# Kernel optimization log

Hardware: AMD Instinct MI355X
Metric: run time of the kernel (lower is better)

The kernel has to match this reference:

```python
import jax, jax.numpy as jnp
import numpy as np

TAU = 0.07
MARGIN = 0.2
NUM_SPECIES = 64  # matches fill_max of species_ids


def _l2norm(x):
    return x / jnp.linalg.norm(x, axis=-1, keepdims=True)


def setup_inputs() -> dict:
    key = jax.random.key(0)
    k1, k2, k3 = jax.random.split(key, 3)
    B, D = 8192, 256
    species_embed = _l2norm(jax.random.normal(k1, (B, D), dtype=jnp.float32))
    text_embed = _l2norm(jax.random.normal(k2, (B, D), dtype=jnp.float32))
    species_ids = jax.random.randint(k3, (B,), 0, NUM_SPECIES, dtype=jnp.int32)
    return {"species_embed": species_embed, "text_embed": text_embed,
            "species_ids": species_ids}


def reference(species_embed, text_embed, species_ids):
    B = species_embed.shape[0]
    dtype = species_embed.dtype

    sim = species_embed @ text_embed.T                      # (B, B)
    same = species_ids[:, None] == species_ids[None, :]     # (B, B) bool, symmetric
    diag_sim = jnp.diagonal(sim)                            # (B,)

    # ---- intra-species symmetric InfoNCE (per-species CE, averaged over species)
    logits = sim / TAU
    neg_inf = jnp.finfo(dtype).min
    masked = jnp.where(same, logits, neg_inf)               # restrict to same-species cols
    diag_logit = diag_sim / TAU
    ce_v2t = jax.scipy.special.logsumexp(masked, axis=1) - diag_logit   # per-row CE
    ce_t2v = jax.scipy.special.logsumexp(masked.T, axis=1) - diag_logit # transpose: same mask is symmetric

    ones = jnp.ones((B,), dtype=dtype)
    counts = jax.ops.segment_sum(ones, species_ids, num_segments=NUM_SPECIES)          # group sizes
    seg_v2t = jax.ops.segment_sum(ce_v2t, species_ids, num_segments=NUM_SPECIES)
    seg_t2v = jax.ops.segment_sum(ce_t2v, species_ids, num_segments=NUM_SPECIES)
    valid_s = counts >= 2                                   # groups with <2 members skipped
    per_species = (seg_v2t + seg_t2v) / (2.0 * jnp.maximum(counts, 1.0))
    n_valid = jnp.maximum(jnp.sum(valid_s.astype(dtype)), 1.0)
    loss_infonce = jnp.sum(jnp.where(valid_s, per_species, 0.0)) / n_valid

    # ---- cross-species triplet (pos = mean same-species sim excl. self, neg = mean diff-species sim)
    same_f = same.astype(dtype)
    row_same_sum = jnp.sum(sim * same_f, axis=1)            # includes diagonal
    row_sum = jnp.sum(sim, axis=1)
    pos_cnt = jnp.sum(same_f, axis=1) - 1.0
    neg_cnt = B - jnp.sum(same_f, axis=1)
    pos_mean = (row_same_sum - diag_sim) / jnp.maximum(pos_cnt, 1.0)
    neg_mean = (row_sum - row_same_sum) / jnp.maximum(neg_cnt, 1.0)
    tri = jax.nn.relu(neg_mean - pos_mean + MARGIN)
    valid_i = (pos_cnt > 0) & (neg_cnt > 0)
    n_valid_i = jnp.maximum(jnp.sum(valid_i.astype(dtype)), 1.0)
    loss_triplet = jnp.sum(jnp.where(valid_i, tri, 0.0)) / n_valid_i

    return loss_infonce + loss_triplet
```

## Files before the change

kernel.cpp:

```cpp
#include <hip/hip_runtime.h>
#include <hip/hip_fp16.h>

#define TAU 0.07f
#define MARGIN 0.2f
#define NSPEC 64
#define BB 8192
#define DD 256

#define WS_SCALARS   0
#define WS_COUNTS    288
#define WS_OFFSETS   544
#define WS_LSEROW    1024
#define WS_LSECOL    33792
#define WS_TS        66560
#define WS_DIAG      132096
#define WS_MEMBER    164864
#define WS_T         197632
#define WS_TRI       198656
#define WS_ZERO_BYTES 132096

typedef _Float16 half8 __attribute__((ext_vector_type(8)));
typedef float float4v __attribute__((ext_vector_type(4)));
typedef unsigned int uint4v __attribute__((ext_vector_type(4)));

__device__ __forceinline__ uint4v pack8(float4 a, float4 b) {
  half8 h;
  h[0] = (_Float16)a.x; h[1] = (_Float16)a.y; h[2] = (_Float16)a.z; h[3] = (_Float16)a.w;
  h[4] = (_Float16)b.x; h[5] = (_Float16)b.y; h[6] = (_Float16)b.z; h[7] = (_Float16)b.w;
  return __builtin_bit_cast(uint4v, h);
}

__global__ void k1_all(const int* __restrict__ ids, int* counts_g, int* offsets_g,
                       int* memberList, float* scalars) {
  __shared__ int cnt[NSPEC];
  __shared__ int off[NSPEC];
  int tid = threadIdx.x;
  if (tid < NSPEC) cnt[tid] = 0;
  __syncthreads();
  int myS[8], myP[8];
  #pragma unroll
  for (int r = 0; r < 8; ++r) {
    int i = r * 1024 + tid;
    int s = ids[i];
    myS[r] = s;
    myP[r] = atomicAdd(&cnt[s], 1);
  }
  __syncthreads();
  if (tid < NSPEC) {
    int o = 0;
    for (int t = 0; t < NSPEC; ++t) o += (t < tid) ? cnt[t] : 0;
    off[tid] = o;
    offsets_g[tid] = o;
    int c = cnt[tid];
    counts_g[tid] = c;
    unsigned long long bv = __ballot(c >= 2);
    float nvi = (c >= 2 && c <= BB - 1) ? (float)c : 0.f;
    for (int o2 = 1; o2 < 64; o2 <<= 1) nvi += __shfl_xor(nvi, o2);
    if (tid == 0) {
      scalars[2] = (float)__popcll(bv);
      scalars[3] = nvi;
    }
  }
  __syncthreads();
  #pragma unroll
  for (int r = 0; r < 8; ++r) {
    int i = r * 1024 + tid;
    memberList[off[myS[r]] + myP[r]] = i;
  }
}

__global__ void k2_ts(const float* __restrict__ tx, const int* __restrict__ counts,
                      const int* __restrict__ offsets, const int* __restrict__ memberList,
                      float* Ts) {
  int s = blockIdx.x, r = blockIdx.y;
  int m = counts[s], g0 = offsets[s];
  int k0 = (m * r) >> 3, k1 = (m * (r + 1)) >> 3;
  if (k0 >= k1) return;
  int d = threadIdx.x;
  float acc = 0.f;
  for (int k = k0; k < k1; ++k) acc += tx[memberList[g0 + k] * DD + d];
  atomicAdd(&Ts[s * DD + d], acc);
}

__global__ void k2b_t(const float* __restrict__ Ts, float* T) {
  int d = threadIdx.x;
  float acc = 0.f;
  for (int s = 0; s < NSPEC; ++s) acc += Ts[s * DD + d];
  T[d] = acc;
}

__global__ void k4_rows(const float* __restrict__ sp, const float* __restrict__ tx,
                        const int* __restrict__ ids, const int* __restrict__ counts,
                        const float* __restrict__ Ts, const float* __restrict__ T,
                        float* diag, float* tri) {
  int gt = blockIdx.x * 256 + threadIdx.x;
  int i = gt >> 6, lane = gt & 63;
  float4 a = *reinterpret_cast<const float4*>(sp + i * DD + lane * 4);
  float4 b = *reinterpret_cast<const float4*>(tx + i * DD + lane * 4);
  float4 tv = *reinterpret_cast<const float4*>(T + lane * 4);
  int s = ids[i];
  int m = counts[s];
  float4 c = *reinterpret_cast<const float4*>(Ts + s * DD + lane * 4);
  float dDiag = a.x * b.x + a.y * b.y + a.z * b.z + a.w * b.w;
  float dT    = a.x * tv.x + a.y * tv.y + a.z * tv.z + a.w * tv.w;
  float dTs   = a.x * c.x + a.y * c.y + a.z * c.z + a.w * c.w;
  #pragma unroll
  for (int o = 1; o < 64; o <<= 1) {
    dDiag += __shfl_xor(dDiag, o);
    dT    += __shfl_xor(dT, o);
    dTs   += __shfl_xor(dTs, o);
  }
  if (lane == 0) {
    diag[i] = dDiag;
    float posMean = (dTs - dDiag) / fmaxf((float)(m - 1), 1.f);
    float negMean = (dT - dTs) / fmaxf((float)(BB - m), 1.f);
    float t = fmaxf(negMean - posMean + MARGIN, 0.f);
    tri[i] = (m >= 2 && m <= BB - 1) ? t : 0.f;
  }
}

__global__ void k5_lse(const float* __restrict__ sp, const float* __restrict__ tx,
                       const int* __restrict__ counts, const int* __restrict__ offsets,
                       const int* __restrict__ memberList,
                       float* lseRow, float* lseCol) {
  __shared__ uint4v lds5[1536];
  int s = blockIdx.x;
  int m = counts[s];
  int g0 = offsets[s];
  int tid = threadIdx.x;
  int lane = tid & 63, wv = tid >> 6;
  int quad = lane >> 4, cl = lane & 15;

  for (int rt = blockIdx.y; rt * 64 < m; rt += gridDim.y) {
    for (int ct = blockIdx.z; ct * 128 < m; ct += gridDim.z) {
      float4v acc[8];
      #pragma unroll
      for (int cf = 0; cf < 8; ++cf) acc[cf] = (float4v){0.f, 0.f, 0.f, 0.f};

      for (int kc = 0; kc < 4; ++kc) {
        __syncthreads();
        #pragma unroll
        for (int p = 0; p < 6; ++p) {
          int u = p * 256 + tid;
          int isB = u >= 512;
          int v = isB ? (u - 512) : u;
          int row = v >> 3;
          int sub = v & 7;
          int ksl = sub >> 2, q = sub & 3;
          int d0 = kc * 64 + ksl * 32 + q * 8;
          int idx = isB ? (ct * 128 + row) : (rt * 64 + row);
          uint4v val = (uint4v){0u, 0u, 0u, 0u};
          if (idx < m) {
            const float* src = (isB ? tx : sp) + memberList[g0 + idx] * DD + d0;
            float4 f0 = *reinterpret_cast<const float4*>(src);
            float4 f1 = *reinterpret_cast<const float4*>(src + 4);
            val = pack8(f0, f1);
          }
          int dst = isB ? (512 + (ksl * 128 + row) * 4 + q)
                        : ((ksl * 64 + row) * 4 + q);
          lds5[dst] = val;
        }
        __syncthreads();
        #pragma unroll
        for (int ksl = 0; ksl < 2; ++ksl) {
          half8 a = __builtin_bit_cast(half8, lds5[(ksl * 64 + wv * 16 + cl) * 4 + quad]);
          #pragma unroll
          for (int cf = 0; cf < 8; ++cf) {
            half8 b = __builtin_bit_cast(half8, lds5[512 + (ksl * 128 + cf * 16 + cl) * 4 + quad]);
            acc[cf] = __builtin_amdgcn_mfma_f32_16x16x32_f16(a, b, acc[cf], 0, 0, 0);
          }
        }
      }

      int riBase = rt * 64 + wv * 16 + quad * 4;
      float rowAcc[4] = {0.f, 0.f, 0.f, 0.f};
      #pragma unroll
      for (int cf = 0; cf < 8; ++cf) {
        int ci = ct * 128 + cf * 16 + cl;
        bool cv = ci < m;
        float colAcc = 0.f;
        #pragma unroll
        for (int reg = 0; reg < 4; ++reg) {
          bool rv = (riBase + reg) < m;
          float e = (rv && cv) ? __expf(acc[cf][reg] * (1.f / TAU)) : 0.f;
          rowAcc[reg] += e;
          colAcc += e;
        }
        colAcc += __shfl_xor(colAcc, 16);
        colAcc += __shfl_xor(colAcc, 32);
        if (quad == 0 && cv) atomicAdd(&lseCol[g0 + ci], colAcc);
      }
      #pragma unroll
      for (int reg = 0; reg < 4; ++reg) {
        float v = rowAcc[reg];
        v += __shfl_xor(v, 1);
        v += __shfl_xor(v, 2);
        v += __shfl_xor(v, 4);
        v += __shfl_xor(v, 8);
        if (cl == 0 && (riBase + reg) < m) atomicAdd(&lseRow[g0 + riBase + reg], v);
      }
    }
  }
}

__global__ void k6_info(const int* __restrict__ memberList, const int* __restrict__ ids,
                        const int* __restrict__ counts, const float* __restrict__ lseRow,
                        const float* __restrict__ lseCol, const float* __restrict__ diag,
                        const float* __restrict__ tri, float* scalars) {
  __shared__ float red[8];
  int g = blockIdx.x * blockDim.x + threadIdx.x;
  int i = memberList[g];
  int s = ids[i];
  int m = counts[s];
  float tt = tri[i];
  float term = 0.f;
  if (m >= 2) {
    term = (__logf(lseRow[g]) + __logf(lseCol[g]) - 2.f * diag[i] * (1.f / TAU)) /
           (2.f * (float)m);
  }
  #pragma unroll
  for (int o = 1; o < 64; o <<= 1) {
    term += __shfl_xor(term, o);
    tt += __shfl_xor(tt, o);
  }
  int wv = threadIdx.x >> 6, lane = threadIdx.x & 63;
  if (lane == 0) { red[wv] = term; red[4 + wv] = tt; }
  __syncthreads();
  if (threadIdx.x == 0) {
    atomicAdd(&scalars[1], red[0] + red[1] + red[2] + red[3]);
    atomicAdd(&scalars[0], red[4] + red[5] + red[6] + red[7]);
  }
}

__global__ void k7_final(const float* __restrict__ scalars, float* out) {
  out[0] = scalars[1] / fmaxf(scalars[2], 1.f) + scalars[0] / fmaxf(scalars[3], 1.f);
}

extern "C" void kernel_launch(void* const* d_in, const int* in_sizes, int n_in,
                              void* d_out, int out_size, void* d_ws, size_t ws_size,
                              hipStream_t stream) {
  const float* sp = (const float*)d_in[0];
  const float* tx = (const float*)d_in[1];
  const int* ids = (const int*)d_in[2];
  float* out = (float*)d_out;

  char* ws = (char*)d_ws;
  float* scalars = (float*)(ws + WS_SCALARS);
  int* counts = (int*)(ws + WS_COUNTS);
  int* offsets = (int*)(ws + WS_OFFSETS);
  float* lseRow = (float*)(ws + WS_LSEROW);
  float* lseCol = (float*)(ws + WS_LSECOL);
  float* Ts = (float*)(ws + WS_TS);
  float* diag = (float*)(ws + WS_DIAG);
  int* memberList = (int*)(ws + WS_MEMBER);
  float* T = (float*)(ws + WS_T);
  float* tri = (float*)(ws + WS_TRI);

  hipMemsetAsync(d_ws, 0, WS_ZERO_BYTES, stream);
  k1_all<<<1, 1024, 0, stream>>>(ids, counts, offsets, memberList, scalars);
  k2_ts<<<dim3(NSPEC, 8), 256, 0, stream>>>(tx, counts, offsets, memberList, Ts);
  k2b_t<<<1, 256, 0, stream>>>(Ts, T);
  k4_rows<<<BB / 4, 256, 0, stream>>>(sp, tx, ids, counts, Ts, T, diag, tri);
  k5_lse<<<dim3(NSPEC, 4, 2), 256, 0, stream>>>(sp, tx, counts, offsets, memberList,
                                                lseRow, lseCol);
  k6_info<<<32, 256, 0, stream>>>(memberList, ids, counts, lseRow, lseCol, diag, tri,
                                  scalars);
  k7_final<<<1, 1, 0, stream>>>(scalars, out);
}
```

Baseline: 111.0 us.

## Fuse pipeline stages to cut kernel launches and the workspace memset

The workspace zeroing moves into the single-block k1 kernel, replacing the separate memset. The total-sum kernel is folded into k2_ts via atomic adds into T. The row-stats kernel and the LSE tile kernel are merged into one heterogeneous grid, with the LSE part remapped onto 128 blocks. The final scalar combine now runs in the last-arriving block of the info kernel through an atomic counter. This removes several launches and inter-kernel gaps, at the cost of extra global atomics and a serial zero-fill done by one block.

```diff
diff --git a/kernel.cpp b/kernel.cpp
--- a/kernel.cpp
+++ b/kernel.cpp
@@ -13,15 +13,18 @@
 #define WS_LSEROW    1024
 #define WS_LSECOL    33792
 #define WS_TS        66560
-#define WS_DIAG      132096
-#define WS_MEMBER    164864
-#define WS_T         197632
-#define WS_TRI       198656
-#define WS_ZERO_BYTES 132096
+#define WS_T         132096
+#define WS_ZERO_BYTES 133120
+#define WS_DIAG      133632
+#define WS_MEMBER    166400
+#define WS_TRI       199168
 
 typedef _Float16 half8 __attribute__((ext_vector_type(8)));
 typedef float float4v __attribute__((ext_vector_type(4)));
 typedef unsigned int uint4v __attribute__((ext_vector_type(4)));
+
+#define NB5 128
+#define NB45 (NB5 + BB/4)
 
 __device__ __forceinline__ uint4v pack8(float4 a, float4 b) {
   half8 h;
@@ -30,11 +33,14 @@
   return __builtin_bit_cast(uint4v, h);
 }
 
-__global__ void k1_all(const int* __restrict__ ids, int* counts_g, int* offsets_g,
-                       int* memberList, float* scalars) {
+__global__ void k1_all(const int* __restrict__ ids, char* ws, int* counts_g,
+                       int* offsets_g, int* memberList, float* scalars) {
   __shared__ int cnt[NSPEC];
   __shared__ int off[NSPEC];
   int tid = threadIdx.x;
+  float4* z = (float4*)ws;
+  float4 z4 = make_float4(0.f, 0.f, 0.f, 0.f);
+  for (int u = tid; u < WS_ZERO_BYTES / 16; u += 1024) z[u] = z4;
   if (tid < NSPEC) cnt[tid] = 0;
   __syncthreads();
   int myS[8], myP[8];
@@ -71,7 +77,7 @@
 
 __global__ void k2_ts(const float* __restrict__ tx, const int* __restrict__ counts,
                       const int* __restrict__ offsets, const int* __restrict__ memberList,
-                      float* Ts) {
+                      float* Ts, float* T) {
   int s = blockIdx.x, r = blockIdx.y;
   int m = counts[s], g0 = offsets[s];
   int k0 = (m * r) >> 3, k1 = (m * (r + 1)) >> 3;
@@ -80,59 +86,54 @@
   float acc = 0.f;
   for (int k = k0; k < k1; ++k) acc += tx[memberList[g0 + k] * DD + d];
   atomicAdd(&Ts[s * DD + d], acc);
-}
-
-__global__ void k2b_t(const float* __restrict__ Ts, float* T) {
-  int d = threadIdx.x;
-  float acc = 0.f;
-  for (int s = 0; s < NSPEC; ++s) acc += Ts[s * DD + d];
-  T[d] = acc;
-}
-
-__global__ void k4_rows(const float* __restrict__ sp, const float* __restrict__ tx,
-                        const int* __restrict__ ids, const int* __restrict__ counts,
-                        const float* __restrict__ Ts, const float* __restrict__ T,
-                        float* diag, float* tri) {
-  int gt = blockIdx.x * 256 + threadIdx.x;
-  int i = gt >> 6, lane = gt & 63;
-  float4 a = *reinterpret_cast<const float4*>(sp + i * DD + lane * 4);
-  float4 b = *reinterpret_cast<const float4*>(tx + i * DD + lane * 4);
-  float4 tv = *reinterpret_cast<const float4*>(T + lane * 4);
-  int s = ids[i];
-  int m = counts[s];
-  float4 c = *reinterpret_cast<const float4*>(Ts + s * DD + lane * 4);
-  float dDiag = a.x * b.x + a.y * b.y + a.z * b.z + a.w * b.w;
-  float dT    = a.x * tv.x + a.y * tv.y + a.z * tv.z + a.w * tv.w;
-  float dTs   = a.x * c.x + a.y * c.y + a.z * c.z + a.w * c.w;
-  #pragma unroll
-  for (int o = 1; o < 64; o <<= 1) {
-    dDiag += __shfl_xor(dDiag, o);
-    dT    += __shfl_xor(dT, o);
-    dTs   += __shfl_xor(dTs, o);
-  }
-  if (lane == 0) {
-    diag[i] = dDiag;
-    float posMean = (dTs - dDiag) / fmaxf((float)(m - 1), 1.f);
-    float negMean = (dT - dTs) / fmaxf((float)(BB - m), 1.f);
-    float t = fmaxf(negMean - posMean + MARGIN, 0.f);
-    tri[i] = (m >= 2 && m <= BB - 1) ? t : 0.f;
-  }
-}
-
-__global__ void k5_lse(const float* __restrict__ sp, const float* __restrict__ tx,
-                       const int* __restrict__ counts, const int* __restrict__ offsets,
-                       const int* __restrict__ memberList,
-                       float* lseRow, float* lseCol) {
+  atomicAdd(&T[d], acc);
+}
+
+__global__ void k45(const float* __restrict__ sp, const float* __restrict__ tx,
+                    const int* __restrict__ ids, const int* __restrict__ counts,
+                    const int* __restrict__ offsets, const int* __restrict__ memberList,
+                    const float* __restrict__ Ts, const float* __restrict__ T,
+                    float* diag, float* tri, float* lseRow, float* lseCol) {
   __shared__ uint4v lds5[1536];
-  int s = blockIdx.x;
+  int tid = threadIdx.x;
+
+  if (blockIdx.x >= NB5) {
+    int gt = (blockIdx.x - NB5) * 256 + tid;
+    int i = gt >> 6, lane = gt & 63;
+    float4 a = *reinterpret_cast<const float4*>(sp + i * DD + lane * 4);
+    float4 b = *reinterpret_cast<const float4*>(tx + i * DD + lane * 4);
+    float4 tv = *reinterpret_cast<const float4*>(T + lane * 4);
+    int s = ids[i];
+    int m = counts[s];
+    float4 c = *reinterpret_cast<const float4*>(Ts + s * DD + lane * 4);
+    float dDiag = a.x * b.x + a.y * b.y + a.z * b.z + a.w * b.w;
+    float dT    = a.x * tv.x + a.y * tv.y + a.z * tv.z + a.w * tv.w;
+    float dTs   = a.x * c.x + a.y * c.y + a.z * c.z + a.w * c.w;
+    #pragma unroll
+    for (int o = 1; o < 64; o <<= 1) {
+      dDiag += __shfl_xor(dDiag, o);
+      dT    += __shfl_xor(dT, o);
+      dTs   += __shfl_xor(dTs, o);
+    }
+    if (lane == 0) {
+      diag[i] = dDiag;
+      float posMean = (dTs - dDiag) / fmaxf((float)(m - 1), 1.f);
+      float negMean = (dT - dTs) / fmaxf((float)(BB - m), 1.f);
+      float t = fmaxf(negMean - posMean + MARGIN, 0.f);
+      tri[i] = (m >= 2 && m <= BB - 1) ? t : 0.f;
+    }
+    return;
+  }
+
+  int s = blockIdx.x >> 1;
+  int rt0 = blockIdx.x & 1;
   int m = counts[s];
   int g0 = offsets[s];
-  int tid = threadIdx.x;
   int lane = tid & 63, wv = tid >> 6;
   int quad = lane >> 4, cl = lane & 15;
 
-  for (int rt = blockIdx.y; rt * 64 < m; rt += gridDim.y) {
-    for (int ct = blockIdx.z; ct * 128 < m; ct += gridDim.z) {
+  for (int rt = rt0; rt * 64 < m; rt += 2) {
+    for (int ct = 0; ct * 128 < m; ++ct) {
       float4v acc[8];
       #pragma unroll
       for (int cf = 0; cf < 8; ++cf) acc[cf] = (float4v){0.f, 0.f, 0.f, 0.f};
@@ -203,10 +204,10 @@
   }
 }
 
-__global__ void k6_info(const int* __restrict__ memberList, const int* __restrict__ ids,
-                        const int* __restrict__ counts, const float* __restrict__ lseRow,
-                        const float* __restrict__ lseCol, const float* __restrict__ diag,
-                        const float* __restrict__ tri, float* scalars) {
+__global__ void k67_info(const int* __restrict__ memberList, const int* __restrict__ ids,
+                         const int* __restrict__ counts, const float* __restrict__ lseRow,
+                         const float* __restrict__ lseCol, const float* __restrict__ diag,
+                         const float* __restrict__ tri, float* scalars, float* out) {
   __shared__ float red[8];
   int g = blockIdx.x * blockDim.x + threadIdx.x;
   int i = memberList[g];
@@ -229,11 +230,14 @@
   if (threadIdx.x == 0) {
     atomicAdd(&scalars[1], red[0] + red[1] + red[2] + red[3]);
     atomicAdd(&scalars[0], red[4] + red[5] + red[6] + red[7]);
-  }
-}
-
-__global__ void k7_final(const float* __restrict__ scalars, float* out) {
-  out[0] = scalars[1] / fmaxf(scalars[2], 1.f) + scalars[0] / fmaxf(scalars[3], 1.f);
+    __threadfence();
+    int old = atomicAdd((int*)&scalars[4], 1);
+    if (old == (int)gridDim.x - 1) {
+      float info = atomicAdd(&scalars[1], 0.f);
+      float trs  = atomicAdd(&scalars[0], 0.f);
+      out[0] = info / fmaxf(scalars[2], 1.f) + trs / fmaxf(scalars[3], 1.f);
+    }
+  }
 }
 
 extern "C" void kernel_launch(void* const* d_in, const int* in_sizes, int n_in,
@@ -251,19 +255,15 @@
   float* lseRow = (float*)(ws + WS_LSEROW);
   float* lseCol = (float*)(ws + WS_LSECOL);
   float* Ts = (float*)(ws + WS_TS);
+  float* T = (float*)(ws + WS_T);
   float* diag = (float*)(ws + WS_DIAG);
   int* memberList = (int*)(ws + WS_MEMBER);
-  float* T = (float*)(ws + WS_T);
   float* tri = (float*)(ws + WS_TRI);
 
-  hipMemsetAsync(d_ws, 0, WS_ZERO_BYTES, stream);
-  k1_all<<<1, 1024, 0, stream>>>(ids, counts, offsets, memberList, scalars);
-  k2_ts<<<dim3(NSPEC, 8), 256, 0, stream>>>(tx, counts, offsets, memberList, Ts);
-  k2b_t<<<1, 256, 0, stream>>>(Ts, T);
-  k4_rows<<<BB / 4, 256, 0, stream>>>(sp, tx, ids, counts, Ts, T, diag, tri);
-  k5_lse<<<dim3(NSPEC, 4, 2), 256, 0, stream>>>(sp, tx, counts, offsets, memberList,
-                                                lseRow, lseCol);
-  k6_info<<<32, 256, 0, stream>>>(memberList, ids, counts, lseRow, lseCol, diag, tri,
-                                  scalars);
-  k7_final<<<1, 1, 0, stream>>>(scalars, out);
-}
+  k1_all<<<1, 1024, 0, stream>>>(ids, ws, counts, offsets, memberList, scalars);
+  k2_ts<<<dim3(NSPEC, 8), 256, 0, stream>>>(tx, counts, offsets, memberList, Ts, T);
+  k45<<<NB45, 256, 0, stream>>>(sp, tx, ids, counts, offsets, memberList, Ts, T,
+                                diag, tri, lseRow, lseCol);
+  k67_info<<<BB / 256, 256, 0, stream>>>(memberList, ids, counts, lseRow, lseCol,
+                                         diag, tri, scalars, out);
+}
```

After: 139.8 us. +25.9%, slower.
